# Kernel optimization log

Measured on AMD Instinct MI355X. Metric: run time of the kernel, lower is better.

Reference implementation:

```python
import jax, jax.numpy as jnp
import numpy as np


def setup_inputs() -> dict:
    key = jax.random.key(0)
    k1, k2, k3, k4 = jax.random.split(key, 4)
    B, H, W, D, C = 1, 20, 20, 20, 64
    x = jax.random.normal(k1, (B, H, W, D, C), dtype=jnp.float32)
    Wb = jax.random.normal(k2, (C, C // 8), dtype=jnp.float32) * 0.05
    Wc = jax.random.normal(k3, (C, C // 8), dtype=jnp.float32) * 0.05
    Wd = jax.random.normal(k4, (C, C), dtype=jnp.float32) * 0.05
    gamma = jnp.zeros((1,), dtype=jnp.float32) + 0.5  # nonzero so attention branch matters
    return {"x": x, "Wb": Wb, "Wc": Wc, "Wd": Wd, "gamma": gamma}


def reference(x, Wb, Wc, Wd, gamma):
    B, H, W, D, C = x.shape
    N = H * W * D
    xf = x.reshape(B, N, C)                       # [B, N, C]
    # 1x1x1 convs (no bias) == per-token dense projections
    b = xf @ Wb                                   # keys    [B, N, C//8]
    c = xf @ Wc                                   # queries [B, N, C//8]
    v = xf @ Wd                                   # values  [B, N, C]
    # scores[i, j] = c_i . b_j  (no 1/sqrt(dk) scaling, matching original)
    scores = jnp.einsum('bnk,bmk->bnm', c, b)     # [B, N, N]
    attn = jax.nn.softmax(scores, axis=-1)
    ctx = jnp.einsum('bnm,bmc->bnc', attn, v)     # [B, N, C]
    out = gamma * ctx + xf
    return out.reshape(B, H, W, D, C)
```

## Files before the change

kernel.cpp:

```cpp
#include <hip/hip_runtime.h>
#include <hip/hip_bf16.h>

typedef __attribute__((ext_vector_type(8))) short short8;
typedef __attribute__((ext_vector_type(16))) float f32x16;
typedef __attribute__((ext_vector_type(4))) float fx4;
typedef __attribute__((ext_vector_type(4))) unsigned uint4v;

#define LOG2E_F 1.4426950408889634f

#define KB_OFF   0u
#define CQ_OFF   65536u
#define VF_OFF   131072u
#define PACC_F   524288u
#define PLS_F    2621440u

__device__ __forceinline__ float fast_exp2(float v) {
#if __has_builtin(__builtin_amdgcn_exp2f)
    return __builtin_amdgcn_exp2f(v);
#else
    return exp2f(v);
#endif
}

__device__ __forceinline__ unsigned short f2bfu(float f) {
    unsigned short u;
    __hip_bfloat16 h = __float2bfloat16(f);
    __builtin_memcpy(&u, &h, 2);
    return u;
}

__device__ __forceinline__ unsigned pk2(float lo, float hi) {
    return (unsigned)f2bfu(lo) | ((unsigned)f2bfu(hi) << 16);
}

__device__ __forceinline__ short8 cvt8(fx4 a, fx4 b) {
    uint4v u;
    u[0] = pk2(a[0], a[1]);
    u[1] = pk2(a[2], a[3]);
    u[2] = pk2(b[0], b[1]);
    u[3] = pk2(b[2], b[3]);
    return __builtin_bit_cast(short8, u);
}

__global__ __launch_bounds__(256, 1) void pam_proj(
    const float* __restrict__ x,
    const float* __restrict__ Wb,
    const float* __restrict__ Wc,
    const float* __restrict__ Wd,
    unsigned short* __restrict__ ws)
{
    __shared__ alignas(16) unsigned short Wt[96][72];

    const int tid = threadIdx.x;
#pragma unroll
    for (int i = 0; i < 24; ++i) {
        int e = tid + 256 * i;
        int col = e >> 6, k = e & 63;
        float w;
        if (col < 8)       w = Wb[k * 8 + col];
        else if (col < 16) w = Wc[k * 8 + (col - 8)] * LOG2E_F;
        else if (col < 80) w = Wd[k * 64 + (col - 16)];
        else               w = 0.0f;
        Wt[col][k] = f2bfu(w);
    }
    __syncthreads();

    const int wave = tid >> 6, lane = tid & 63;
    const int l31 = lane & 31, g = lane >> 5;
    const int rowbase = blockIdx.x * 128 + wave * 32;
    if (rowbase >= 8000) return;

    short8 bfrag[3][4];
#pragma unroll
    for (int ct = 0; ct < 3; ++ct)
#pragma unroll
        for (int kk = 0; kk < 4; ++kk)
            bfrag[ct][kk] = *reinterpret_cast<const short8*>(&Wt[ct * 32 + l31][kk * 16 + g * 8]);

    const float* xr = x + (size_t)(rowbase + l31) * 64 + g * 8;
    short8 afrag[4];
#pragma unroll
    for (int kk = 0; kk < 4; ++kk) {
        fx4 a = *reinterpret_cast<const fx4*>(xr + kk * 16);
        fx4 b = *reinterpret_cast<const fx4*>(xr + kk * 16 + 4);
        afrag[kk] = cvt8(a, b);
    }

    f32x16 acc[3] = {};
#pragma unroll
    for (int kk = 0; kk < 4; ++kk) {
#pragma unroll
        for (int ct = 0; ct < 3; ++ct)
            acc[ct] = __builtin_amdgcn_mfma_f32_32x32x16_bf16(afrag[kk], bfrag[ct][kk], acc[ct], 0, 0, 0);
    }

#pragma unroll
    for (int ct = 0; ct < 3; ++ct) {
        const int col = ct * 32 + l31;
#pragma unroll
        for (int r = 0; r < 16; ++r) {
            const int row = rowbase + (r & 3) + 8 * (r >> 2) + 4 * g;
            const unsigned short hv = f2bfu(acc[ct][r]);
            if (col < 8) {
                ws[KB_OFF + row * 8u + col] = hv;
            } else if (col < 16) {
                ws[CQ_OFF + row * 8u + (col - 8)] = hv;
            } else if (col < 80) {
                const unsigned j  = col - 16;
                const unsigned t5 = row & 31u;
                const unsigned ks = t5 >> 4;
                const unsigned rr = t5 & 15u;
                const unsigned gg = (rr >> 2) & 1u;
                const unsigned ee = (rr & 3u) + ((rr >> 3) << 2);
                ws[VF_OFF + (row >> 5) * 2048u + ks * 1024u + gg * 512u + j * 8u + ee] = hv;
            }
        }
    }
}

__global__ __launch_bounds__(256, 4) void pam_attn(
    const unsigned short* __restrict__ ws,
    float* __restrict__ wsf)
{
    __shared__ alignas(16) float acc_s[4][32][64];
    __shared__ float ls_s[4][2][32];

    const int tid  = threadIdx.x;
    const int wave = tid >> 6;
    const int lane = tid & 63;
    const int l31  = lane & 31;
    const int g    = lane >> 5;
    const int qt   = blockIdx.x >> 2;
    const int kp   = blockIdx.x & 3;
    const int qbase = qt * 32;

    const short8* kbp = reinterpret_cast<const short8*>(ws + KB_OFF);
    const short8* cqp = reinterpret_cast<const short8*>(ws + CQ_OFF);
    const short8* vp  = reinterpret_cast<const short8*>(ws + VF_OFF);

    short8 cf = {};
    if (lane < 32) cf = cqp[qbase + l31];

    f32x16 acc0 = {};
    f32x16 acc1 = {};
    float ls0 = 0.f, ls1 = 0.f, ls2 = 0.f, ls3 = 0.f;

    const int plen   = (kp < 2) ? 63 : 62;
    const int pstart = kp * 62 + ((kp < 2) ? kp : 2);
    const int s0 = pstart + (plen * wave) / 4;
    const int s1 = pstart + (plen * (wave + 1)) / 4;

    short8 kf = {};
    if (lane < 32) kf = kbp[s0 * 32 + l31];
    const int vb = s0 * 256 + g * 64 + l31;
    short8 v00 = vp[vb];
    short8 v01 = vp[vb + 32];
    short8 v10 = vp[vb + 128];
    short8 v11 = vp[vb + 160];

    for (int s = s0; s < s1; ++s) {
        const int sn = s + 1;
        short8 kfn = {};
        short8 n00 = {}, n01 = {}, n10 = {}, n11 = {};
        if (sn < s1) {
            if (lane < 32) kfn = kbp[sn * 32 + l31];
            const int nb = sn * 256 + g * 64 + l31;
            n00 = vp[nb];
            n01 = vp[nb + 32];
            n10 = vp[nb + 128];
            n11 = vp[nb + 160];
        }

        f32x16 z = {};
        f32x16 st = __builtin_amdgcn_mfma_f32_32x32x16_bf16(kf, cf, z, 0, 0, 0);

        float e[16];
#pragma unroll
        for (int r = 0; r < 16; ++r) e[r] = fast_exp2(st[r]);

        ls0 += (e[0]  + e[1])  + (e[2]  + e[3]);
        ls1 += (e[4]  + e[5])  + (e[6]  + e[7]);
        ls2 += (e[8]  + e[9])  + (e[10] + e[11]);
        ls3 += (e[12] + e[13]) + (e[14] + e[15]);

        uint4v u0, u1;
#pragma unroll
        for (int p = 0; p < 4; ++p) u0[p] = pk2(e[2 * p], e[2 * p + 1]);
#pragma unroll
        for (int p = 0; p < 4; ++p) u1[p] = pk2(e[8 + 2 * p], e[9 + 2 * p]);
        const short8 af0 = __builtin_bit_cast(short8, u0);
        const short8 af1 = __builtin_bit_cast(short8, u1);

        acc0 = __builtin_amdgcn_mfma_f32_32x32x16_bf16(af0, v00, acc0, 0, 0, 0);
        acc1 = __builtin_amdgcn_mfma_f32_32x32x16_bf16(af0, v01, acc1, 0, 0, 0);
        acc0 = __builtin_amdgcn_mfma_f32_32x32x16_bf16(af1, v10, acc0, 0, 0, 0);
        acc1 = __builtin_amdgcn_mfma_f32_32x32x16_bf16(af1, v11, acc1, 0, 0, 0);

        kf = kfn; v00 = n00; v01 = n01; v10 = n10; v11 = n11;
    }

    ls_s[wave][g][l31] = (ls0 + ls1) + (ls2 + ls3);
#pragma unroll
    for (int r = 0; r < 16; ++r) {
        const int row = (r & 3) + 8 * (r >> 2) + 4 * g;
        acc_s[wave][row][l31]      = acc0[r];
        acc_s[wave][row][32 + l31] = acc1[r];
    }
    __syncthreads();

    if (tid < 32) {
        float s = 0.f;
#pragma unroll
        for (int w = 0; w < 4; ++w) s += ls_s[w][0][tid] + ls_s[w][1][tid];
        wsf[PLS_F + blockIdx.x * 32u + tid] = s;
    }
    const int q = tid >> 3, j0 = (tid & 7) * 8;
    fx4 a0 = {}, a1 = {};
#pragma unroll
    for (int w = 0; w < 4; ++w) {
        a0 += *reinterpret_cast<const fx4*>(&acc_s[w][q][j0]);
        a1 += *reinterpret_cast<const fx4*>(&acc_s[w][q][j0 + 4]);
    }
    float* pb = wsf + PACC_F + (size_t)blockIdx.x * 2048u + q * 64 + j0;
    *reinterpret_cast<fx4*>(pb)     = a0;
    *reinterpret_cast<fx4*>(pb + 4) = a1;
}

__global__ __launch_bounds__(256) void pam_merge(
    const float* __restrict__ x,
    const float* __restrict__ gamma_p,
    const float* __restrict__ wsf,
    float* __restrict__ out)
{
    const int tid = threadIdx.x;
    const int qt  = blockIdx.x;
    const int q = tid >> 3, j0 = (tid & 7) * 8;

    float lq = 0.f;
#pragma unroll
    for (int p = 0; p < 4; ++p) lq += wsf[PLS_F + (qt * 4 + p) * 32u + q];
    const float sc = gamma_p[0] / lq;

    fx4 a0 = {}, a1 = {};
#pragma unroll
    for (int p = 0; p < 4; ++p) {
        const float* pb = wsf + PACC_F + (size_t)(qt * 4 + p) * 2048u + q * 64 + j0;
        a0 += *reinterpret_cast<const fx4*>(pb);
        a1 += *reinterpret_cast<const fx4*>(pb + 4);
    }

    const int base = (qt * 32 + q) * 64 + j0;
    const fx4 x0 = *reinterpret_cast<const fx4*>(x + base);
    const fx4 x1 = *reinterpret_cast<const fx4*>(x + base + 4);
    *reinterpret_cast<fx4*>(out + base)     = a0 * sc + x0;
    *reinterpret_cast<fx4*>(out + base + 4) = a1 * sc + x1;
}

extern "C" void kernel_launch(void* const* d_in, const int* in_sizes, int n_in,
                              void* d_out, int out_size, void* d_ws, size_t ws_size,
                              hipStream_t stream)
{
    const float* x     = (const float*)d_in[0];
    const float* Wb    = (const float*)d_in[1];
    const float* Wc    = (const float*)d_in[2];
    const float* Wd    = (const float*)d_in[3];
    const float* gamma = (const float*)d_in[4];
    float* outp = (float*)d_out;
    unsigned short* ws = (unsigned short*)d_ws;
    float* wsf = (float*)d_ws;

    hipLaunchKernelGGL(pam_proj, dim3(63), dim3(256), 0, stream, x, Wb, Wc, Wd, ws);
    hipLaunchKernelGGL(pam_attn, dim3(1000), dim3(256), 0, stream,
                       (const unsigned short*)ws, wsf);
    hipLaunchKernelGGL(pam_merge, dim3(250), dim3(256), 0, stream,
                       x, gamma, (const float*)wsf, outp);
}
```

Measured before the change: 35.52 us.

## Process 64 queries per wave, split keys 16 ways, store bf16 partials

The attention kernel now has each wave handle two 32-query tiles over one of 16 key partitions, reusing each K/V load for twice the queries. It drops the shared-memory cross-wave reduction and writes per-wave partial accumulators to global memory packed as bf16, which halves partial-store traffic. The merge kernel sums 16 partials instead of 4, and the projection kernel is relaunched with 128-thread blocks and coalesced weight loading. This costs more merge reads, lower occupancy (launch bound 2), and extra rounding error from storing the partials in bf16.

```diff
diff --git a/kernel.cpp b/kernel.cpp
--- a/kernel.cpp
+++ b/kernel.cpp
@@ -11,8 +11,8 @@
 #define KB_OFF   0u
 #define CQ_OFF   65536u
 #define VF_OFF   131072u
-#define PACC_F   524288u
-#define PLS_F    2621440u
+#define PLS_F    524288u
+#define PACC_U   1048576u
 
 __device__ __forceinline__ float fast_exp2(float v) {
 #if __has_builtin(__builtin_amdgcn_exp2f)
@@ -42,7 +42,7 @@
     return __builtin_bit_cast(short8, u);
 }
 
-__global__ __launch_bounds__(256, 1) void pam_proj(
+__global__ __launch_bounds__(128, 1) void pam_proj(
     const float* __restrict__ x,
     const float* __restrict__ Wb,
     const float* __restrict__ Wc,
@@ -53,22 +53,28 @@
 
     const int tid = threadIdx.x;
 #pragma unroll
-    for (int i = 0; i < 24; ++i) {
-        int e = tid + 256 * i;
-        int col = e >> 6, k = e & 63;
-        float w;
-        if (col < 8)       w = Wb[k * 8 + col];
-        else if (col < 16) w = Wc[k * 8 + (col - 8)] * LOG2E_F;
-        else if (col < 80) w = Wd[k * 64 + (col - 16)];
-        else               w = 0.0f;
-        Wt[col][k] = f2bfu(w);
+    for (int i = 0; i < 32; ++i) {
+        int e = i * 128 + tid;
+        int col = e & 63, k = e >> 6;
+        Wt[16 + col][k] = f2bfu(Wd[k * 64 + col]);
+    }
+#pragma unroll
+    for (int i = 0; i < 8; ++i) {
+        int e = i * 128 + tid;
+        int c = e & 15, k = e >> 4;
+        float w = (c < 8) ? Wb[k * 8 + c] : Wc[k * 8 + (c - 8)] * LOG2E_F;
+        Wt[c][k] = f2bfu(w);
+    }
+#pragma unroll
+    for (int i = 0; i < 9; ++i) {
+        int e = i * 128 + tid;
+        if (e < 1152) Wt[80 + e / 72][e - (e / 72) * 72] = 0;
     }
     __syncthreads();
 
     const int wave = tid >> 6, lane = tid & 63;
     const int l31 = lane & 31, g = lane >> 5;
-    const int rowbase = blockIdx.x * 128 + wave * 32;
-    if (rowbase >= 8000) return;
+    const int rowbase = blockIdx.x * 64 + wave * 32;
 
     short8 bfrag[3][4];
 #pragma unroll
@@ -88,11 +94,10 @@
 
     f32x16 acc[3] = {};
 #pragma unroll
-    for (int kk = 0; kk < 4; ++kk) {
+    for (int kk = 0; kk < 4; ++kk)
 #pragma unroll
         for (int ct = 0; ct < 3; ++ct)
             acc[ct] = __builtin_amdgcn_mfma_f32_32x32x16_bf16(afrag[kk], bfrag[ct][kk], acc[ct], 0, 0, 0);
-    }
 
 #pragma unroll
     for (int ct = 0; ct < 3; ++ct) {
@@ -118,37 +123,36 @@
     }
 }
 
-__global__ __launch_bounds__(256, 4) void pam_attn(
+__global__ __launch_bounds__(256, 2) void pam_attn(
     const unsigned short* __restrict__ ws,
-    float* __restrict__ wsf)
+    float* __restrict__ wsf,
+    unsigned* __restrict__ wsu)
 {
-    __shared__ alignas(16) float acc_s[4][32][64];
-    __shared__ float ls_s[4][2][32];
-
     const int tid  = threadIdx.x;
     const int wave = tid >> 6;
     const int lane = tid & 63;
     const int l31  = lane & 31;
     const int g    = lane >> 5;
-    const int qt   = blockIdx.x >> 2;
-    const int kp   = blockIdx.x & 3;
-    const int qbase = qt * 32;
+    const int kp   = blockIdx.x & 15;
+    const int qt   = (blockIdx.x >> 4) * 4 + wave;
+    if (qt >= 125) return;
+    const int qbase = qt * 64;
 
     const short8* kbp = reinterpret_cast<const short8*>(ws + KB_OFF);
     const short8* cqp = reinterpret_cast<const short8*>(ws + CQ_OFF);
     const short8* vp  = reinterpret_cast<const short8*>(ws + VF_OFF);
 
-    short8 cf = {};
-    if (lane < 32) cf = cqp[qbase + l31];
-
-    f32x16 acc0 = {};
-    f32x16 acc1 = {};
-    float ls0 = 0.f, ls1 = 0.f, ls2 = 0.f, ls3 = 0.f;
-
-    const int plen   = (kp < 2) ? 63 : 62;
-    const int pstart = kp * 62 + ((kp < 2) ? kp : 2);
-    const int s0 = pstart + (plen * wave) / 4;
-    const int s1 = pstart + (plen * (wave + 1)) / 4;
+    short8 cf0 = {}, cf1 = {};
+    if (lane < 32) {
+        cf0 = cqp[qbase + l31];
+        cf1 = cqp[qbase + 32 + l31];
+    }
+
+    f32x16 acc00 = {}, acc01 = {}, acc10 = {}, acc11 = {};
+    float ls0 = 0.f, ls1 = 0.f;
+
+    const int s0 = (250 * kp) >> 4;
+    const int s1 = (250 * (kp + 1)) >> 4;
 
     short8 kf = {};
     if (lane < 32) kf = kbp[s0 * 32 + l31];
@@ -172,88 +176,117 @@
         }
 
         f32x16 z = {};
-        f32x16 st = __builtin_amdgcn_mfma_f32_32x32x16_bf16(kf, cf, z, 0, 0, 0);
-
-        float e[16];
-#pragma unroll
-        for (int r = 0; r < 16; ++r) e[r] = fast_exp2(st[r]);
-
-        ls0 += (e[0]  + e[1])  + (e[2]  + e[3]);
-        ls1 += (e[4]  + e[5])  + (e[6]  + e[7]);
-        ls2 += (e[8]  + e[9])  + (e[10] + e[11]);
-        ls3 += (e[12] + e[13]) + (e[14] + e[15]);
-
-        uint4v u0, u1;
-#pragma unroll
-        for (int p = 0; p < 4; ++p) u0[p] = pk2(e[2 * p], e[2 * p + 1]);
-#pragma unroll
-        for (int p = 0; p < 4; ++p) u1[p] = pk2(e[8 + 2 * p], e[9 + 2 * p]);
-        const short8 af0 = __builtin_bit_cast(short8, u0);
-        const short8 af1 = __builtin_bit_cast(short8, u1);
-
-        acc0 = __builtin_amdgcn_mfma_f32_32x32x16_bf16(af0, v00, acc0, 0, 0, 0);
-        acc1 = __builtin_amdgcn_mfma_f32_32x32x16_bf16(af0, v01, acc1, 0, 0, 0);
-        acc0 = __builtin_amdgcn_mfma_f32_32x32x16_bf16(af1, v10, acc0, 0, 0, 0);
-        acc1 = __builtin_amdgcn_mfma_f32_32x32x16_bf16(af1, v11, acc1, 0, 0, 0);
+        const f32x16 st0 = __builtin_amdgcn_mfma_f32_32x32x16_bf16(kf, cf0, z, 0, 0, 0);
+        const f32x16 st1 = __builtin_amdgcn_mfma_f32_32x32x16_bf16(kf, cf1, z, 0, 0, 0);
+
+        {
+            float e[16];
+#pragma unroll
+            for (int r = 0; r < 16; ++r) e[r] = fast_exp2(st0[r]);
+            ls0 += ((e[0] + e[1]) + (e[2] + e[3])) + ((e[4] + e[5]) + (e[6] + e[7]))
+                 + ((e[8] + e[9]) + (e[10] + e[11])) + ((e[12] + e[13]) + (e[14] + e[15]));
+            uint4v u0, u1;
+#pragma unroll
+            for (int p = 0; p < 4; ++p) u0[p] = pk2(e[2 * p], e[2 * p + 1]);
+#pragma unroll
+            for (int p = 0; p < 4; ++p) u1[p] = pk2(e[8 + 2 * p], e[9 + 2 * p]);
+            const short8 af0 = __builtin_bit_cast(short8, u0);
+            const short8 af1 = __builtin_bit_cast(short8, u1);
+            acc00 = __builtin_amdgcn_mfma_f32_32x32x16_bf16(af0, v00, acc00, 0, 0, 0);
+            acc01 = __builtin_amdgcn_mfma_f32_32x32x16_bf16(af0, v01, acc01, 0, 0, 0);
+            acc00 = __builtin_amdgcn_mfma_f32_32x32x16_bf16(af1, v10, acc00, 0, 0, 0);
+            acc01 = __builtin_amdgcn_mfma_f32_32x32x16_bf16(af1, v11, acc01, 0, 0, 0);
+        }
+        {
+            float e[16];
+#pragma unroll
+            for (int r = 0; r < 16; ++r) e[r] = fast_exp2(st1[r]);
+            ls1 += ((e[0] + e[1]) + (e[2] + e[3])) + ((e[4] + e[5]) + (e[6] + e[7]))
+                 + ((e[8] + e[9]) + (e[10] + e[11])) + ((e[12] + e[13]) + (e[14] + e[15]));
+            uint4v u0, u1;
+#pragma unroll
+            for (int p = 0; p < 4; ++p) u0[p] = pk2(e[2 * p], e[2 * p + 1]);
+#pragma unroll
+            for (int p = 0; p < 4; ++p) u1[p] = pk2(e[8 + 2 * p], e[9 + 2 * p]);
+            const short8 af0 = __builtin_bit_cast(short8, u0);
+            const short8 af1 = __builtin_bit_cast(short8, u1);
+            acc10 = __builtin_amdgcn_mfma_f32_32x32x16_bf16(af0, v00, acc10, 0, 0, 0);
+            acc11 = __builtin_amdgcn_mfma_f32_32x32x16_bf16(af0, v01, acc11, 0, 0, 0);
+            acc10 = __builtin_amdgcn_mfma_f32_32x32x16_bf16(af1, v10, acc10, 0, 0, 0);
+            acc11 = __builtin_amdgcn_mfma_f32_32x32x16_bf16(af1, v11, acc11, 0, 0, 0);
+        }
 
         kf = kfn; v00 = n00; v01 = n01; v10 = n10; v11 = n11;
     }
 
-    ls_s[wave][g][l31] = (ls0 + ls1) + (ls2 + ls3);
+    const unsigned lsbase = ((unsigned)qt * 16u + kp) * 128u;
+    wsf[PLS_F + lsbase +       g * 32u + l31] = ls0;
+    wsf[PLS_F + lsbase + 64u + g * 32u + l31] = ls1;
+
+    const unsigned pbase = ((unsigned)qt * 16u + kp) * 64u;
 #pragma unroll
     for (int r = 0; r < 16; ++r) {
-        const int row = (r & 3) + 8 * (r >> 2) + 4 * g;
-        acc_s[wave][row][l31]      = acc0[r];
-        acc_s[wave][row][32 + l31] = acc1[r];
-    }
-    __syncthreads();
-
-    if (tid < 32) {
-        float s = 0.f;
-#pragma unroll
-        for (int w = 0; w < 4; ++w) s += ls_s[w][0][tid] + ls_s[w][1][tid];
-        wsf[PLS_F + blockIdx.x * 32u + tid] = s;
-    }
-    const int q = tid >> 3, j0 = (tid & 7) * 8;
-    fx4 a0 = {}, a1 = {};
-#pragma unroll
-    for (int w = 0; w < 4; ++w) {
-        a0 += *reinterpret_cast<const fx4*>(&acc_s[w][q][j0]);
-        a1 += *reinterpret_cast<const fx4*>(&acc_s[w][q][j0 + 4]);
-    }
-    float* pb = wsf + PACC_F + (size_t)blockIdx.x * 2048u + q * 64 + j0;
-    *reinterpret_cast<fx4*>(pb)     = a0;
-    *reinterpret_cast<fx4*>(pb + 4) = a1;
+        const int q0 = (r & 3) + 8 * (r >> 2) + 4 * g;
+        wsu[PACC_U + (pbase + q0) * 32u + l31]        = pk2(acc00[r], acc01[r]);
+        wsu[PACC_U + (pbase + 32 + q0) * 32u + l31]   = pk2(acc10[r], acc11[r]);
+    }
 }
 
 __global__ __launch_bounds__(256) void pam_merge(
     const float* __restrict__ x,
     const float* __restrict__ gamma_p,
     const float* __restrict__ wsf,
+    const unsigned* __restrict__ wsu,
     float* __restrict__ out)
 {
     const int tid = threadIdx.x;
     const int qt  = blockIdx.x;
-    const int q = tid >> 3, j0 = (tid & 7) * 8;
+    const int q   = tid >> 2;
+    const int i0  = (tid & 3) * 8;
+    const int qgrp = q >> 5, qi = q & 31;
 
     float lq = 0.f;
 #pragma unroll
-    for (int p = 0; p < 4; ++p) lq += wsf[PLS_F + (qt * 4 + p) * 32u + q];
+    for (int kp = 0; kp < 16; ++kp) {
+        const unsigned lb = PLS_F + ((unsigned)(qt * 16 + kp)) * 128u + qgrp * 64u + qi;
+        lq += wsf[lb] + wsf[lb + 32];
+    }
+
+    float alo[8] = {}, ahi[8] = {};
+#pragma unroll
+    for (int kp = 0; kp < 16; ++kp) {
+        const unsigned* pb = wsu + PACC_U + (((unsigned)(qt * 16 + kp)) * 64u + q) * 32u + i0;
+        const uint4v w0 = *reinterpret_cast<const uint4v*>(pb);
+        const uint4v w1 = *reinterpret_cast<const uint4v*>(pb + 4);
+#pragma unroll
+        for (int t = 0; t < 4; ++t) {
+            alo[t]     += __builtin_bit_cast(float, w0[t] << 16);
+            ahi[t]     += __builtin_bit_cast(float, w0[t] & 0xffff0000u);
+            alo[4 + t] += __builtin_bit_cast(float, w1[t] << 16);
+            ahi[4 + t] += __builtin_bit_cast(float, w1[t] & 0xffff0000u);
+        }
+    }
+
     const float sc = gamma_p[0] / lq;
-
-    fx4 a0 = {}, a1 = {};
-#pragma unroll
-    for (int p = 0; p < 4; ++p) {
-        const float* pb = wsf + PACC_F + (size_t)(qt * 4 + p) * 2048u + q * 64 + j0;
-        a0 += *reinterpret_cast<const fx4*>(pb);
-        a1 += *reinterpret_cast<const fx4*>(pb + 4);
-    }
-
-    const int base = (qt * 32 + q) * 64 + j0;
-    const fx4 x0 = *reinterpret_cast<const fx4*>(x + base);
-    const fx4 x1 = *reinterpret_cast<const fx4*>(x + base + 4);
-    *reinterpret_cast<fx4*>(out + base)     = a0 * sc + x0;
-    *reinterpret_cast<fx4*>(out + base + 4) = a1 * sc + x1;
+    const int base = (qt * 64 + q) * 64;
+
+    fx4 o;
+#pragma unroll
+    for (int h = 0; h < 2; ++h) {
+        const int off = base + i0 + 4 * h;
+        const fx4 xr = *reinterpret_cast<const fx4*>(x + off);
+#pragma unroll
+        for (int t = 0; t < 4; ++t) o[t] = alo[4 * h + t] * sc + xr[t];
+        *reinterpret_cast<fx4*>(out + off) = o;
+    }
+#pragma unroll
+    for (int h = 0; h < 2; ++h) {
+        const int off = base + 32 + i0 + 4 * h;
+        const fx4 xr = *reinterpret_cast<const fx4*>(x + off);
+#pragma unroll
+        for (int t = 0; t < 4; ++t) o[t] = ahi[4 * h + t] * sc + xr[t];
+        *reinterpret_cast<fx4*>(out + off) = o;
+    }
 }
 
 extern "C" void kernel_launch(void* const* d_in, const int* in_sizes, int n_in,
@@ -268,10 +301,11 @@
     float* outp = (float*)d_out;
     unsigned short* ws = (unsigned short*)d_ws;
     float* wsf = (float*)d_ws;
-
-    hipLaunchKernelGGL(pam_proj, dim3(63), dim3(256), 0, stream, x, Wb, Wc, Wd, ws);
-    hipLaunchKernelGGL(pam_attn, dim3(1000), dim3(256), 0, stream,
-                       (const unsigned short*)ws, wsf);
-    hipLaunchKernelGGL(pam_merge, dim3(250), dim3(256), 0, stream,
-                       x, gamma, (const float*)wsf, outp);
-}
+    unsigned* wsu = (unsigned*)d_ws;
+
+    hipLaunchKernelGGL(pam_proj, dim3(125), dim3(128), 0, stream, x, Wb, Wc, Wd, ws);
+    hipLaunchKernelGGL(pam_attn, dim3(512), dim3(256), 0, stream,
+                       (const unsigned short*)ws, wsf, wsu);
+    hipLaunchKernelGGL(pam_merge, dim3(125), dim3(256), 0, stream,
+                       x, gamma, (const float*)wsf, (const unsigned*)wsu, outp);
+}
```

Result: slower. 40.98 us (+15.4%).

## Split attention keys 32 ways per wave, write bf16 partials, merge globally

Applied to the files above, without the earlier changes.

Each attention block now gives its four waves four different query tiles that share the same key slice. The keys are split into 32 slices, where before a block covered one query tile with 4 key partitions. The in-block LDS reduction and the barrier are gone: every wave writes its partial context straight to the workspace, packed as bf16 pairs, along with its row sums. The merge kernel then reduces 32 partials per query tile. The loop prefetch is now unconditional, clamping to the last slice so the branch disappears. The projection kernel moves to 128-thread blocks, with a coalesced weight transpose and no early exit. The trade-offs are more partial-result traffic and bf16 rounding of the partial sums.

```diff
diff --git a/kernel.cpp b/kernel.cpp
--- a/kernel.cpp
+++ b/kernel.cpp
@@ -11,8 +11,8 @@
 #define KB_OFF   0u
 #define CQ_OFF   65536u
 #define VF_OFF   131072u
-#define PACC_F   524288u
-#define PLS_F    2621440u
+#define PLS_F    524288u
+#define PACC_U   1048576u
 
 __device__ __forceinline__ float fast_exp2(float v) {
 #if __has_builtin(__builtin_amdgcn_exp2f)
@@ -42,7 +42,7 @@
     return __builtin_bit_cast(short8, u);
 }
 
-__global__ __launch_bounds__(256, 1) void pam_proj(
+__global__ __launch_bounds__(128, 1) void pam_proj(
     const float* __restrict__ x,
     const float* __restrict__ Wb,
     const float* __restrict__ Wc,
@@ -53,22 +53,28 @@
 
     const int tid = threadIdx.x;
 #pragma unroll
-    for (int i = 0; i < 24; ++i) {
-        int e = tid + 256 * i;
-        int col = e >> 6, k = e & 63;
-        float w;
-        if (col < 8)       w = Wb[k * 8 + col];
-        else if (col < 16) w = Wc[k * 8 + (col - 8)] * LOG2E_F;
-        else if (col < 80) w = Wd[k * 64 + (col - 16)];
-        else               w = 0.0f;
-        Wt[col][k] = f2bfu(w);
+    for (int i = 0; i < 32; ++i) {
+        int e = i * 128 + tid;
+        int col = e & 63, k = e >> 6;
+        Wt[16 + col][k] = f2bfu(Wd[k * 64 + col]);
+    }
+#pragma unroll
+    for (int i = 0; i < 8; ++i) {
+        int e = i * 128 + tid;
+        int c = e & 15, k = e >> 4;
+        float w = (c < 8) ? Wb[k * 8 + c] : Wc[k * 8 + (c - 8)] * LOG2E_F;
+        Wt[c][k] = f2bfu(w);
+    }
+#pragma unroll
+    for (int i = 0; i < 9; ++i) {
+        int e = i * 128 + tid;
+        if (e < 1152) Wt[80 + e / 72][e - (e / 72) * 72] = 0;
     }
     __syncthreads();
 
     const int wave = tid >> 6, lane = tid & 63;
     const int l31 = lane & 31, g = lane >> 5;
-    const int rowbase = blockIdx.x * 128 + wave * 32;
-    if (rowbase >= 8000) return;
+    const int rowbase = blockIdx.x * 64 + wave * 32;
 
     short8 bfrag[3][4];
 #pragma unroll
@@ -88,11 +94,10 @@
 
     f32x16 acc[3] = {};
 #pragma unroll
-    for (int kk = 0; kk < 4; ++kk) {
+    for (int kk = 0; kk < 4; ++kk)
 #pragma unroll
         for (int ct = 0; ct < 3; ++ct)
             acc[ct] = __builtin_amdgcn_mfma_f32_32x32x16_bf16(afrag[kk], bfrag[ct][kk], acc[ct], 0, 0, 0);
-    }
 
 #pragma unroll
     for (int ct = 0; ct < 3; ++ct) {
@@ -120,18 +125,18 @@
 
 __global__ __launch_bounds__(256, 4) void pam_attn(
     const unsigned short* __restrict__ ws,
-    float* __restrict__ wsf)
-{
-    __shared__ alignas(16) float acc_s[4][32][64];
-    __shared__ float ls_s[4][2][32];
-
+    float* __restrict__ wsf,
+    unsigned* __restrict__ wsu)
+{
     const int tid  = threadIdx.x;
     const int wave = tid >> 6;
     const int lane = tid & 63;
     const int l31  = lane & 31;
     const int g    = lane >> 5;
-    const int qt   = blockIdx.x >> 2;
-    const int kp   = blockIdx.x & 3;
+    const int qg   = blockIdx.x >> 5;
+    const int kpw  = blockIdx.x & 31;
+    const int qt   = qg * 4 + wave;
+    if (qt >= 250) return;
     const int qbase = qt * 32;
 
     const short8* kbp = reinterpret_cast<const short8*>(ws + KB_OFF);
@@ -141,38 +146,32 @@
     short8 cf = {};
     if (lane < 32) cf = cqp[qbase + l31];
 
-    f32x16 acc0 = {};
-    f32x16 acc1 = {};
+    f32x16 acc0 = {}, acc1 = {};
     float ls0 = 0.f, ls1 = 0.f, ls2 = 0.f, ls3 = 0.f;
 
-    const int plen   = (kp < 2) ? 63 : 62;
-    const int pstart = kp * 62 + ((kp < 2) ? kp : 2);
-    const int s0 = pstart + (plen * wave) / 4;
-    const int s1 = pstart + (plen * (wave + 1)) / 4;
+    const int s0 = (250 * kpw) >> 5;
+    const int s1 = (250 * (kpw + 1)) >> 5;
 
     short8 kf = {};
     if (lane < 32) kf = kbp[s0 * 32 + l31];
-    const int vb = s0 * 256 + g * 64 + l31;
-    short8 v00 = vp[vb];
-    short8 v01 = vp[vb + 32];
-    short8 v10 = vp[vb + 128];
-    short8 v11 = vp[vb + 160];
+    const int vb0 = s0 * 256 + g * 64 + l31;
+    short8 v00 = vp[vb0];
+    short8 v01 = vp[vb0 + 32];
+    short8 v10 = vp[vb0 + 128];
+    short8 v11 = vp[vb0 + 160];
 
     for (int s = s0; s < s1; ++s) {
-        const int sn = s + 1;
+        const int sc = (s + 1 < s1) ? (s + 1) : (s1 - 1);
         short8 kfn = {};
-        short8 n00 = {}, n01 = {}, n10 = {}, n11 = {};
-        if (sn < s1) {
-            if (lane < 32) kfn = kbp[sn * 32 + l31];
-            const int nb = sn * 256 + g * 64 + l31;
-            n00 = vp[nb];
-            n01 = vp[nb + 32];
-            n10 = vp[nb + 128];
-            n11 = vp[nb + 160];
-        }
+        if (lane < 32) kfn = kbp[sc * 32 + l31];
+        const int nb = sc * 256 + g * 64 + l31;
+        const short8 n00 = vp[nb];
+        const short8 n01 = vp[nb + 32];
+        const short8 n10 = vp[nb + 128];
+        const short8 n11 = vp[nb + 160];
 
         f32x16 z = {};
-        f32x16 st = __builtin_amdgcn_mfma_f32_32x32x16_bf16(kf, cf, z, 0, 0, 0);
+        const f32x16 st = __builtin_amdgcn_mfma_f32_32x32x16_bf16(kf, cf, z, 0, 0, 0);
 
         float e[16];
 #pragma unroll
@@ -199,61 +198,62 @@
         kf = kfn; v00 = n00; v01 = n01; v10 = n10; v11 = n11;
     }
 
-    ls_s[wave][g][l31] = (ls0 + ls1) + (ls2 + ls3);
+    const unsigned pw = (unsigned)qt * 32u + (unsigned)kpw;
+    wsf[PLS_F + pw * 64u + g * 32u + l31] = (ls0 + ls1) + (ls2 + ls3);
+
+    const unsigned pb = PACC_U + pw * 1024u;
 #pragma unroll
     for (int r = 0; r < 16; ++r) {
-        const int row = (r & 3) + 8 * (r >> 2) + 4 * g;
-        acc_s[wave][row][l31]      = acc0[r];
-        acc_s[wave][row][32 + l31] = acc1[r];
-    }
-    __syncthreads();
-
-    if (tid < 32) {
-        float s = 0.f;
-#pragma unroll
-        for (int w = 0; w < 4; ++w) s += ls_s[w][0][tid] + ls_s[w][1][tid];
-        wsf[PLS_F + blockIdx.x * 32u + tid] = s;
-    }
-    const int q = tid >> 3, j0 = (tid & 7) * 8;
-    fx4 a0 = {}, a1 = {};
-#pragma unroll
-    for (int w = 0; w < 4; ++w) {
-        a0 += *reinterpret_cast<const fx4*>(&acc_s[w][q][j0]);
-        a1 += *reinterpret_cast<const fx4*>(&acc_s[w][q][j0 + 4]);
-    }
-    float* pb = wsf + PACC_F + (size_t)blockIdx.x * 2048u + q * 64 + j0;
-    *reinterpret_cast<fx4*>(pb)     = a0;
-    *reinterpret_cast<fx4*>(pb + 4) = a1;
+        const int q0 = (r & 3) + 8 * (r >> 2) + 4 * g;
+        wsu[pb + (unsigned)q0 * 32u + l31] = pk2(acc0[r], acc1[r]);
+    }
 }
 
 __global__ __launch_bounds__(256) void pam_merge(
     const float* __restrict__ x,
     const float* __restrict__ gamma_p,
     const float* __restrict__ wsf,
+    const unsigned* __restrict__ wsu,
     float* __restrict__ out)
 {
     const int tid = threadIdx.x;
     const int qt  = blockIdx.x;
-    const int q = tid >> 3, j0 = (tid & 7) * 8;
+    const int q   = tid >> 3;
+    const int i0  = (tid & 7) * 4;
 
     float lq = 0.f;
 #pragma unroll
-    for (int p = 0; p < 4; ++p) lq += wsf[PLS_F + (qt * 4 + p) * 32u + q];
+    for (int kpw = 0; kpw < 32; ++kpw) {
+        const unsigned lb = PLS_F + ((unsigned)(qt * 32 + kpw)) * 64u + q;
+        lq += wsf[lb] + wsf[lb + 32];
+    }
+
+    fx4 alo = {}, ahi = {};
+#pragma unroll
+    for (int kpw = 0; kpw < 32; ++kpw) {
+        const unsigned* pb = wsu + PACC_U
+            + (((unsigned)(qt * 32 + kpw)) * 32u + q) * 32u + i0;
+        const uint4v w = *reinterpret_cast<const uint4v*>(pb);
+#pragma unroll
+        for (int t = 0; t < 4; ++t) {
+            alo[t] += __builtin_bit_cast(float, w[t] << 16);
+            ahi[t] += __builtin_bit_cast(float, w[t] & 0xffff0000u);
+        }
+    }
+
     const float sc = gamma_p[0] / lq;
-
-    fx4 a0 = {}, a1 = {};
-#pragma unroll
-    for (int p = 0; p < 4; ++p) {
-        const float* pb = wsf + PACC_F + (size_t)(qt * 4 + p) * 2048u + q * 64 + j0;
-        a0 += *reinterpret_cast<const fx4*>(pb);
-        a1 += *reinterpret_cast<const fx4*>(pb + 4);
-    }
-
-    const int base = (qt * 32 + q) * 64 + j0;
-    const fx4 x0 = *reinterpret_cast<const fx4*>(x + base);
-    const fx4 x1 = *reinterpret_cast<const fx4*>(x + base + 4);
-    *reinterpret_cast<fx4*>(out + base)     = a0 * sc + x0;
-    *reinterpret_cast<fx4*>(out + base + 4) = a1 * sc + x1;
+    const int base = (qt * 32 + q) * 64;
+
+    const fx4 x0 = *reinterpret_cast<const fx4*>(x + base + i0);
+    const fx4 x1 = *reinterpret_cast<const fx4*>(x + base + 32 + i0);
+    fx4 o0, o1;
+#pragma unroll
+    for (int t = 0; t < 4; ++t) {
+        o0[t] = alo[t] * sc + x0[t];
+        o1[t] = ahi[t] * sc + x1[t];
+    }
+    *reinterpret_cast<fx4*>(out + base + i0)      = o0;
+    *reinterpret_cast<fx4*>(out + base + 32 + i0) = o1;
 }
 
 extern "C" void kernel_launch(void* const* d_in, const int* in_sizes, int n_in,
@@ -268,10 +268,11 @@
     float* outp = (float*)d_out;
     unsigned short* ws = (unsigned short*)d_ws;
     float* wsf = (float*)d_ws;
-
-    hipLaunchKernelGGL(pam_proj, dim3(63), dim3(256), 0, stream, x, Wb, Wc, Wd, ws);
-    hipLaunchKernelGGL(pam_attn, dim3(1000), dim3(256), 0, stream,
-                       (const unsigned short*)ws, wsf);
+    unsigned* wsu = (unsigned*)d_ws;
+
+    hipLaunchKernelGGL(pam_proj, dim3(125), dim3(128), 0, stream, x, Wb, Wc, Wd, ws);
+    hipLaunchKernelGGL(pam_attn, dim3(2016), dim3(256), 0, stream,
+                       (const unsigned short*)ws, wsf, wsu);
     hipLaunchKernelGGL(pam_merge, dim3(250), dim3(256), 0, stream,
-                       x, gamma, (const float*)wsf, outp);
-}
+                       x, gamma, (const float*)wsf, (const unsigned*)wsu, outp);
+}
```

After: 41.87 us. +17.9%, slower.
